# Optimization experiments

Hardware: AMD Instinct MI355X
Metric: run time of the kernel (lower is better)

The kernel has to match this reference:

```python
import jax, jax.numpy as jnp
import numpy as np

N_NODES = 100000
N_EDGES = 3200000


def setup_inputs() -> dict:
    key = jax.random.key(0)
    ks = jax.random.split(key, 10)
    inp = {
        "x": jax.random.normal(ks[0], (N_NODES, 16), dtype=jnp.float32),
        "edge_index": jax.random.randint(ks[1], (2, N_EDGES), 0, N_NODES, dtype=jnp.int64),
        "W1": jax.random.normal(ks[2], (16, 32), dtype=jnp.float32) * 0.25,
        "b1": jax.random.normal(ks[3], (32,), dtype=jnp.float32) * 0.02,
        "W2": jax.random.normal(ks[4], (32, 32), dtype=jnp.float32) * 0.18,
        "b2": jax.random.normal(ks[5], (32,), dtype=jnp.float32) * 0.02,
        "Wl1": jax.random.normal(ks[6], (32, 32), dtype=jnp.float32) * 0.18,
        "bl1": jax.random.normal(ks[7], (32,), dtype=jnp.float32) * 0.02,
        "Wl4": jax.random.normal(ks[8], (32, 1), dtype=jnp.float32) * 0.18,
        "bl4": jax.random.normal(ks[9], (1,), dtype=jnp.float32) * 0.02,
    }
    return inp


def _gcn_norm(edge_index, n_nodes):
    # PyG GCNConv default: add self-loops, symmetric normalization D^-1/2 A_hat D^-1/2.
    loops = jnp.arange(n_nodes, dtype=edge_index.dtype)
    row = jnp.concatenate([edge_index[0], loops])  # source j
    col = jnp.concatenate([edge_index[1], loops])  # target i
    deg = jax.ops.segment_sum(jnp.ones_like(col, dtype=jnp.float32), col, num_segments=n_nodes)
    dinv = jnp.where(deg > 0, jax.lax.rsqrt(deg), 0.0)
    norm = dinv[row] * dinv[col]  # [E + N]
    return row, col, norm


def _gcn_conv(x, W, b, row, col, norm, n_nodes):
    h = x @ W                                   # [N, out] small GEMM
    msgs = h[row] * norm[:, None]               # irregular gather, [E+N, out]
    out = jax.ops.segment_sum(msgs, col, num_segments=n_nodes)  # scatter-add
    return out + b


def reference(x, edge_index, W1, b1, W2, b2, Wl1, bl1, Wl4, bl4):
    n = x.shape[0]
    row, col, norm = _gcn_norm(edge_index, n)
    h = jax.nn.relu(_gcn_conv(x, W1, b1, row, col, norm, n))
    h = jax.nn.relu(_gcn_conv(h, W2, b2, row, col, norm, n))
    h = jax.nn.relu(h @ Wl1 + bl1)
    return h @ Wl4 + bl4  # [N, 1]
```

## Files before the change

### kernel.cpp

```cpp
#include <hip/hip_runtime.h>
#include <hip/hip_fp16.h>
#include <math.h>


#define BN 256
#define BSH 8
#define NBUF 512
#define EPB 4096
#define EPT 8
#define CMAX 10240
#define SLDS 1536

__global__ void __launch_bounds__(512)
bucket_scatter(const int* __restrict__ row, const int* __restrict__ col,
               int* __restrict__ gCursor, int* __restrict__ packed,
               int E, int NB, int C) {
    __shared__ int hist[NBUF];
    __shared__ int base[NBUF];
    int t = threadIdx.x;
    int blockBase = blockIdx.x * EPB;
    for (int i = t; i < NB; i += 512) hist[i] = 0;
    __syncthreads();
    int pay[EPT];
    int meta[EPT];
#pragma unroll
    for (int k = 0; k < EPT; ++k) {
        int e = blockBase + k * 512 + t;
        if (e < E) {
            int c = col[e];
            int b = c >> BSH;
            int r = atomicAdd(&hist[b], 1);
            pay[k] = (row[e] << BSH) | (c & (BN - 1));
            meta[k] = (b << 16) | r;
        } else {
            meta[k] = -1;
        }
    }
    __syncthreads();
    for (int b = t; b < NB; b += 512) {
        int c = hist[b];
        base[b] = c ? atomicAdd(&gCursor[b], c) : 0;
    }
    __syncthreads();
#pragma unroll
    for (int k = 0; k < EPT; ++k) {
        int m = meta[k];
        if (m >= 0) {
            int b = m >> 16;
            int off = base[b] + (m & 0xFFFF);
            if (off < C)
                packed[(size_t)b * C + off] = pay[k];
        }
    }
}

__global__ void __launch_bounds__(1024)
bucket_finalize(const int* __restrict__ packed, const int* __restrict__ gCursor,
                int2* __restrict__ rowRange, int* __restrict__ rowMid,
                float* __restrict__ dinv, int* __restrict__ srcs,
                const float4* __restrict__ x4, __half* __restrict__ xs,
                int N, int C, int halfN) {
    __shared__ int cnt[BN * 2];
    __shared__ int cur[BN * 2];
    __shared__ float sdv[BN];
    __shared__ int wsum[16];
    __shared__ int sorted[CMAX];
    int bkt = blockIdx.x;
    int t = threadIdx.x;
    int nodeBase = bkt << BSH;
    if (t < BN * 2) cnt[t] = 0;
    __syncthreads();
    int beg = bkt * C;
    int end = beg + min(gCursor[bkt], C);
    int m = end - beg;
    for (int e = beg + t; e < end; e += 1024) {
        int w = packed[e];
        int key = ((w & (BN - 1)) << 1) | ((w >> BSH) >= halfN ? 1 : 0);
        atomicAdd(&cnt[key], 1);
    }
    __syncthreads();
    int c0 = (t < BN) ? cnt[2 * t] : 0;
    int c1 = (t < BN) ? cnt[2 * t + 1] : 0;
    int s = c0 + c1;
    int lane = t & 63, wv = t >> 6;
    int v = s;
#pragma unroll
    for (int off = 1; off < 64; off <<= 1) {
        int u = __shfl_up(v, off);
        if (lane >= off) v += u;
    }
    if (lane == 63) wsum[wv] = v;
    __syncthreads();
    int addv = 0;
#pragma unroll
    for (int w = 0; w < 16; ++w) addv += (w < wv) ? wsum[w] : 0;
    v += addv;
    if (t < BN) {
        int p = v - s;
        cur[2 * t] = p;
        cur[2 * t + 1] = p + c0;
        float d = rsqrtf((float)s + 1.0f);
        sdv[t] = d;
        int n = nodeBase + t;
        if (n < N) {
            rowRange[n] = make_int2(beg + p, beg + p + s);
            rowMid[n] = beg + p + c0;
            dinv[n] = d;
        }
    }
    __syncthreads();
    bool useLds = (m <= CMAX);
    for (int e = beg + t; e < end; e += 1024) {
        int w = packed[e];
        int src = w >> BSH;
        int key = ((w & (BN - 1)) << 1) | (src >= halfN ? 1 : 0);
        int pos = atomicAdd(&cur[key], 1);
        if (useLds) sorted[pos] = src;
        else        srcs[beg + pos] = src;
    }
    __syncthreads();
    if (useLds)
        for (int i = t; i < m; i += 1024) srcs[beg + i] = sorted[i];
    {
        int n = t >> 1, hf = t & 1;
        int g = nodeBase + n;
        if (t < BN * 2 && g < N) {
            float d = sdv[n];
            float4 va = x4[(size_t)g * 4 + hf * 2];
            float4 vb = x4[(size_t)g * 4 + hf * 2 + 1];
            __half2 h0 = __floats2half2_rn(va.x * d, va.y * d);
            __half2 h1 = __floats2half2_rn(va.z * d, va.w * d);
            __half2 h2 = __floats2half2_rn(vb.x * d, vb.y * d);
            __half2 h3 = __floats2half2_rn(vb.z * d, vb.w * d);
            uint4 u;
            u.x = *(unsigned*)&h0; u.y = *(unsigned*)&h1;
            u.z = *(unsigned*)&h2; u.w = *(unsigned*)&h3;
            *(uint4*)(xs + (size_t)g * 16 + hf * 8) = u;
        }
    }
}

__device__ __forceinline__ void acc8(float* a, uint4 u) {
    float2 f;
    f = __half22float2(*(const __half2*)&u.x); a[0] += f.x; a[1] += f.y;
    f = __half22float2(*(const __half2*)&u.y); a[2] += f.x; a[3] += f.y;
    f = __half22float2(*(const __half2*)&u.z); a[4] += f.x; a[5] += f.y;
    f = __half22float2(*(const __half2*)&u.w); a[6] += f.x; a[7] += f.y;
}

__device__ __forceinline__ void gather_pipe(float* a, const int* __restrict__ idx,
                                            const __half* __restrict__ tbl,
                                            int rowHalves, int off8,
                                            int first, int limit, int stride) {
    if (first >= limit) return;
    int cntE = (limit - first + stride - 1) / stride;
    int last = limit - 1;
    int i0 = idx[first];
    int i1 = idx[min(first + stride, last)];
    int i2 = idx[min(first + stride * 2, last)];
    int i3 = idx[min(first + stride * 3, last)];
    uint4 f0 = *(const uint4*)(tbl + (size_t)i0 * rowHalves + off8 * 8);
    uint4 f1 = *(const uint4*)(tbl + (size_t)i1 * rowHalves + off8 * 8);
    uint4 f2 = *(const uint4*)(tbl + (size_t)i2 * rowHalves + off8 * 8);
    uint4 f3 = *(const uint4*)(tbl + (size_t)i3 * rowHalves + off8 * 8);
    int i = 0;
    for (; i + 4 <= cntE; i += 4) {
        int n0 = idx[min(first + stride * (i + 4), last)];
        int n1 = idx[min(first + stride * (i + 5), last)];
        int n2 = idx[min(first + stride * (i + 6), last)];
        int n3 = idx[min(first + stride * (i + 7), last)];
        acc8(a, f0); f0 = *(const uint4*)(tbl + (size_t)n0 * rowHalves + off8 * 8);
        acc8(a, f1); f1 = *(const uint4*)(tbl + (size_t)n1 * rowHalves + off8 * 8);
        acc8(a, f2); f2 = *(const uint4*)(tbl + (size_t)n2 * rowHalves + off8 * 8);
        acc8(a, f3); f3 = *(const uint4*)(tbl + (size_t)n3 * rowHalves + off8 * 8);
    }
    int r = cntE - i;
    if (r > 0) acc8(a, f0);
    if (r > 1) acc8(a, f1);
    if (r > 2) acc8(a, f2);
}

__global__ void __launch_bounds__(256)
gather_conv1(const int2* __restrict__ rowRange, const int* __restrict__ srcs,
             const __half* __restrict__ xs, const float* __restrict__ dinv,
             const float* __restrict__ W1, const float* __restrict__ b1,
             __half* __restrict__ hs1, int N) {
    __shared__ float A[32][17];
    __shared__ float sW[512];
    __shared__ float sb[32];
    __shared__ int sIdx[SLDS];
    int t = threadIdx.x;
    for (int i = t; i < 512; i += 256) sW[i] = W1[i];
    if (t < 32) sb[t] = b1[t];
    int node0 = blockIdx.x * 32;
    int lastN = min(node0 + 31, N - 1);
    int base = rowRange[node0].x;
    int tot = rowRange[lastN].y - base;
    bool useLds = (tot <= SLDS);
    if (useLds)
        for (int i = t; i < tot; i += 256) sIdx[i] = srcs[base + i];
    __syncthreads();
    int tt = blockIdx.x * 256 + t;
    int node = tt >> 3, q = tt & 7, ln = t >> 3;
    int eo = q >> 1, hf = q & 1;
    float a[8] = {0.f, 0.f, 0.f, 0.f, 0.f, 0.f, 0.f, 0.f};
    float di = 0.f;
    if (node < N) {
        int2 rr = rowRange[node];
        if (useLds)
            gather_pipe(a, sIdx, xs, 16, hf, rr.x - base + eo, rr.y - base, 4);
        else
            gather_pipe(a, srcs, xs, 16, hf, rr.x + eo, rr.y, 4);
        if (eo == 0)
            acc8(a, *(const uint4*)(xs + (size_t)node * 16 + hf * 8));
        di = dinv[node];
    }
#pragma unroll
    for (int j = 0; j < 8; ++j) {
        a[j] += __shfl_xor(a[j], 2);
        a[j] += __shfl_xor(a[j], 4);
        a[j] *= di;
    }
    if (eo == 0) {
#pragma unroll
        for (int j = 0; j < 8; ++j) A[ln][hf * 8 + j] = a[j];
    }
    __syncthreads();
    if (node < N) {
        int k0 = q * 4;
        float acc[4];
#pragma unroll
        for (int j = 0; j < 4; ++j) acc[j] = sb[k0 + j];
#pragma unroll
        for (int c = 0; c < 16; ++c) {
            float ac = A[ln][c];
#pragma unroll
            for (int j = 0; j < 4; ++j) acc[j] += ac * sW[c * 32 + k0 + j];
        }
        __half2 h0 = __floats2half2_rn(di * fmaxf(acc[0], 0.f),
                                       di * fmaxf(acc[1], 0.f));
        __half2 h1 = __floats2half2_rn(di * fmaxf(acc[2], 0.f),
                                       di * fmaxf(acc[3], 0.f));
        uint2 u;
        u.x = *(unsigned*)&h0; u.y = *(unsigned*)&h1;
        *(uint2*)(hs1 + (size_t)node * 32 + k0) = u;
    }
}

__global__ void __launch_bounds__(256)
gather_conv2_lo(const int2* __restrict__ rowRange, const int* __restrict__ rowMid,
                const int* __restrict__ srcs, const __half* __restrict__ hs1,
                float* __restrict__ A2, int N) {
    __shared__ int sIdx[SLDS];
    int t = threadIdx.x;
    int node0 = blockIdx.x * 32;
    int lastN = min(node0 + 31, N - 1);
    int base = rowRange[node0].x;
    int tot = rowRange[lastN].y - base;
    bool useLds = (tot <= SLDS);
    if (useLds)
        for (int i = t; i < tot; i += 256) sIdx[i] = srcs[base + i];
    __syncthreads();
    int tt = blockIdx.x * 256 + t;
    int node = tt >> 3, q = tt & 7;
    int eo = q >> 2, part = q & 3;
    float a[8] = {0.f, 0.f, 0.f, 0.f, 0.f, 0.f, 0.f, 0.f};
    if (node < N) {
        int beg = rowRange[node].x, mid = rowMid[node];
        if (useLds)
            gather_pipe(a, sIdx, hs1, 32, part, beg - base + eo, mid - base, 2);
        else
            gather_pipe(a, srcs, hs1, 32, part, beg + eo, mid, 2);
    }
#pragma unroll
    for (int j = 0; j < 8; ++j) a[j] += __shfl_xor(a[j], 4);
    if (node < N && eo == 0) {
        float4 r0, r1;
        r0.x = a[0]; r0.y = a[1]; r0.z = a[2]; r0.w = a[3];
        r1.x = a[4]; r1.y = a[5]; r1.z = a[6]; r1.w = a[7];
        *(float4*)(A2 + (size_t)node * 32 + part * 8) = r0;
        *(float4*)(A2 + (size_t)node * 32 + part * 8 + 4) = r1;
    }
}

__global__ void __launch_bounds__(256)
gather_conv2_hi_head(const int2* __restrict__ rowRange, const int* __restrict__ rowMid,
                     const int* __restrict__ srcs, const __half* __restrict__ hs1,
                     const float* __restrict__ A2, const float* __restrict__ dinv,
                     const float* __restrict__ W2, const float* __restrict__ b2,
                     const float* __restrict__ Wl1, const float* __restrict__ bl1,
                     const float* __restrict__ Wl4, const float* __restrict__ bl4,
                     float* __restrict__ out, int N) {
    __shared__ float A[32][33];
    __shared__ float sW2[1024];
    __shared__ float sWl1[1024];
    __shared__ float sb2[32], sbl1[32], sWl4[32];
    __shared__ float sbl4;
    __shared__ int sIdx[SLDS];
    int t = threadIdx.x;
    for (int i = t; i < 1024; i += 256) { sW2[i] = W2[i]; sWl1[i] = Wl1[i]; }
    if (t < 32) { sb2[t] = b2[t]; sbl1[t] = bl1[t]; sWl4[t] = Wl4[t]; }
    if (t == 0) sbl4 = bl4[0];
    int node0 = blockIdx.x * 32;
    int lastN = min(node0 + 31, N - 1);
    int base = rowRange[node0].x;
    int tot = rowRange[lastN].y - base;
    bool useLds = (tot <= SLDS);
    if (useLds)
        for (int i = t; i < tot; i += 256) sIdx[i] = srcs[base + i];
    __syncthreads();
    int tt = blockIdx.x * 256 + t;
    int node = tt >> 3, q = tt & 7, ln = t >> 3;
    int eo = q >> 2, part = q & 3;
    float a[8] = {0.f, 0.f, 0.f, 0.f, 0.f, 0.f, 0.f, 0.f};
    if (node < N) {
        int mid = rowMid[node], end = rowRange[node].y;
        if (useLds)
            gather_pipe(a, sIdx, hs1, 32, part, mid - base + eo, end - base, 2);
        else
            gather_pipe(a, srcs, hs1, 32, part, mid + eo, end, 2);
        if (eo == 0)
            acc8(a, *(const uint4*)(hs1 + (size_t)node * 32 + part * 8));
    }
#pragma unroll
    for (int j = 0; j < 8; ++j) a[j] += __shfl_xor(a[j], 4);
    if (node < N && eo == 0) {
        float4 l0 = *(const float4*)(A2 + (size_t)node * 32 + part * 8);
        float4 l1 = *(const float4*)(A2 + (size_t)node * 32 + part * 8 + 4);
        a[0] += l0.x; a[1] += l0.y; a[2] += l0.z; a[3] += l0.w;
        a[4] += l1.x; a[5] += l1.y; a[6] += l1.z; a[7] += l1.w;
        float di = dinv[node];
#pragma unroll
        for (int j = 0; j < 8; ++j) a[j] *= di;
#pragma unroll
        for (int j = 0; j < 8; ++j) A[ln][part * 8 + j] = a[j];
    }
    __syncthreads();
    int k0 = q * 4;
    float h2[4];
#pragma unroll
    for (int j = 0; j < 4; ++j) h2[j] = sb2[k0 + j];
#pragma unroll
    for (int c = 0; c < 32; ++c) {
        float ac = A[ln][c];
#pragma unroll
        for (int j = 0; j < 4; ++j) h2[j] += ac * sW2[c * 32 + k0 + j];
    }
#pragma unroll
    for (int j = 0; j < 4; ++j) h2[j] = fmaxf(h2[j], 0.f);
    __syncthreads();
#pragma unroll
    for (int j = 0; j < 4; ++j) A[ln][k0 + j] = h2[j];
    __syncthreads();
    float h3[4];
#pragma unroll
    for (int j = 0; j < 4; ++j) h3[j] = sbl1[k0 + j];
#pragma unroll
    for (int c = 0; c < 32; ++c) {
        float ac = A[ln][c];
#pragma unroll
        for (int j = 0; j < 4; ++j) h3[j] += ac * sWl1[c * 32 + k0 + j];
    }
    float p = 0.f;
#pragma unroll
    for (int j = 0; j < 4; ++j) p += fmaxf(h3[j], 0.f) * sWl4[k0 + j];
    p += __shfl_xor(p, 1);
    p += __shfl_xor(p, 2);
    p += __shfl_xor(p, 4);
    if (q == 0 && node < N) out[node] = p + sbl4;
}

extern "C" void kernel_launch(void* const* d_in, const int* in_sizes, int n_in,
                              void* d_out, int out_size, void* d_ws, size_t ws_size,
                              hipStream_t stream) {
    const float* x   = (const float*)d_in[0];
    const int*   ei  = (const int*)d_in[1];
    const float* W1  = (const float*)d_in[2];
    const float* b1  = (const float*)d_in[3];
    const float* W2  = (const float*)d_in[4];
    const float* b2  = (const float*)d_in[5];
    const float* Wl1 = (const float*)d_in[6];
    const float* bl1 = (const float*)d_in[7];
    const float* Wl4 = (const float*)d_in[8];
    const float* bl4 = (const float*)d_in[9];
    float* out = (float*)d_out;

    const int N = in_sizes[0] / 16;
    const int E = in_sizes[1] / 2;
    const int* row = ei;
    const int* col = ei + E;
    const int NB = (N + BN - 1) >> BSH;
    const int halfN = N / 2;
    int C = (E + NB - 1) / NB;
    C = (C * 9 + 7) / 8;
    C = (C + 63) & ~63;

    char* ws = (char*)d_ws;
    auto align = [](size_t v) { return (v + 511) & ~(size_t)511; };
    size_t o = 0;
    int*    gCursor  = (int*)(ws + o);    o = align(o + (size_t)NBUF * 4);
    int2*   rowRange = (int2*)(ws + o);   o = align(o + (size_t)N * 8);
    int*    rowMid   = (int*)(ws + o);    o = align(o + (size_t)N * 4);
    float*  dinv     = (float*)(ws + o);  o = align(o + (size_t)N * 4);
    int*    packed   = (int*)(ws + o);    o = align(o + (size_t)NB * C * 4);
    int*    srcs     = (int*)(ws + o);    o = align(o + (size_t)NB * C * 4);
    __half* xs       = (__half*)(ws + o); o = align(o + (size_t)N * 16 * 2);
    __half* hs1      = (__half*)(ws + o); o = align(o + (size_t)N * 32 * 2);
    float*  A2       = (float*)(ws + o);  o = align(o + (size_t)N * 32 * 4);

    const int BLK = 256;
    int gridSc = (E + EPB - 1) / EPB;
    int gridG8 = (N * 8 + BLK - 1) / BLK;

    hipMemsetAsync(gCursor, 0, (size_t)NBUF * 4, stream);
    bucket_scatter<<<gridSc, 512, 0, stream>>>(row, col, gCursor, packed, E, NB, C);
    bucket_finalize<<<NB, 1024, 0, stream>>>(packed, gCursor, rowRange, rowMid, dinv,
                                             srcs, (const float4*)x, xs, N, C, halfN);

    gather_conv1<<<gridG8, BLK, 0, stream>>>(rowRange, srcs, xs, dinv, W1, b1, hs1, N);

    gather_conv2_lo<<<gridG8, BLK, 0, stream>>>(rowRange, rowMid, srcs, hs1, A2, N);
    gather_conv2_hi_head<<<gridG8, BLK, 0, stream>>>(rowRange, rowMid, srcs, hs1, A2,
                                                     dinv, W2, b2, Wl1, bl1,
                                                     Wl4, bl4, out, N);
}
```

Baseline: 196.6 us.

## Merge split conv2 gather passes into a single fused gather-head kernel

Removes the source-half partitioning of edges within each destination node, along with the rowMid array and the intermediate A2 buffer. Conv2 aggregation now runs in one kernel that gathers all neighbours and applies the MLP head directly. This eliminates a kernel launch, the fp32 partial-sum round trip and the duplicated index loads. The trade-off is that gathers span the whole hs1 feature table instead of half of it at a time, which may reduce L2 cache hit rates.

```diff
diff --git a/kernel.cpp b/kernel.cpp
--- a/kernel.cpp
+++ b/kernel.cpp
@@ -56,32 +56,29 @@
 
 __global__ void __launch_bounds__(1024)
 bucket_finalize(const int* __restrict__ packed, const int* __restrict__ gCursor,
-                int2* __restrict__ rowRange, int* __restrict__ rowMid,
-                float* __restrict__ dinv, int* __restrict__ srcs,
+                int2* __restrict__ rowRange, float* __restrict__ dinv,
+                int* __restrict__ srcs,
                 const float4* __restrict__ x4, __half* __restrict__ xs,
-                int N, int C, int halfN) {
-    __shared__ int cnt[BN * 2];
-    __shared__ int cur[BN * 2];
+                int N, int C) {
+    __shared__ int cnt[BN];
+    __shared__ int cur[BN];
     __shared__ float sdv[BN];
     __shared__ int wsum[16];
     __shared__ int sorted[CMAX];
     int bkt = blockIdx.x;
     int t = threadIdx.x;
     int nodeBase = bkt << BSH;
-    if (t < BN * 2) cnt[t] = 0;
+    if (t < BN) cnt[t] = 0;
     __syncthreads();
     int beg = bkt * C;
     int end = beg + min(gCursor[bkt], C);
     int m = end - beg;
     for (int e = beg + t; e < end; e += 1024) {
         int w = packed[e];
-        int key = ((w & (BN - 1)) << 1) | ((w >> BSH) >= halfN ? 1 : 0);
-        atomicAdd(&cnt[key], 1);
-    }
-    __syncthreads();
-    int c0 = (t < BN) ? cnt[2 * t] : 0;
-    int c1 = (t < BN) ? cnt[2 * t + 1] : 0;
-    int s = c0 + c1;
+        atomicAdd(&cnt[w & (BN - 1)], 1);
+    }
+    __syncthreads();
+    int s = (t < BN) ? cnt[t] : 0;
     int lane = t & 63, wv = t >> 6;
     int v = s;
 #pragma unroll
@@ -97,14 +94,12 @@
     v += addv;
     if (t < BN) {
         int p = v - s;
-        cur[2 * t] = p;
-        cur[2 * t + 1] = p + c0;
+        cur[t] = p;
         float d = rsqrtf((float)s + 1.0f);
         sdv[t] = d;
         int n = nodeBase + t;
         if (n < N) {
             rowRange[n] = make_int2(beg + p, beg + p + s);
-            rowMid[n] = beg + p + c0;
             dinv[n] = d;
         }
     }
@@ -113,8 +108,7 @@
     for (int e = beg + t; e < end; e += 1024) {
         int w = packed[e];
         int src = w >> BSH;
-        int key = ((w & (BN - 1)) << 1) | (src >= halfN ? 1 : 0);
-        int pos = atomicAdd(&cur[key], 1);
+        int pos = atomicAdd(&cur[w & (BN - 1)], 1);
         if (useLds) sorted[pos] = src;
         else        srcs[beg + pos] = src;
     }
@@ -248,49 +242,12 @@
 }
 
 __global__ void __launch_bounds__(256)
-gather_conv2_lo(const int2* __restrict__ rowRange, const int* __restrict__ rowMid,
-                const int* __restrict__ srcs, const __half* __restrict__ hs1,
-                float* __restrict__ A2, int N) {
-    __shared__ int sIdx[SLDS];
-    int t = threadIdx.x;
-    int node0 = blockIdx.x * 32;
-    int lastN = min(node0 + 31, N - 1);
-    int base = rowRange[node0].x;
-    int tot = rowRange[lastN].y - base;
-    bool useLds = (tot <= SLDS);
-    if (useLds)
-        for (int i = t; i < tot; i += 256) sIdx[i] = srcs[base + i];
-    __syncthreads();
-    int tt = blockIdx.x * 256 + t;
-    int node = tt >> 3, q = tt & 7;
-    int eo = q >> 2, part = q & 3;
-    float a[8] = {0.f, 0.f, 0.f, 0.f, 0.f, 0.f, 0.f, 0.f};
-    if (node < N) {
-        int beg = rowRange[node].x, mid = rowMid[node];
-        if (useLds)
-            gather_pipe(a, sIdx, hs1, 32, part, beg - base + eo, mid - base, 2);
-        else
-            gather_pipe(a, srcs, hs1, 32, part, beg + eo, mid, 2);
-    }
-#pragma unroll
-    for (int j = 0; j < 8; ++j) a[j] += __shfl_xor(a[j], 4);
-    if (node < N && eo == 0) {
-        float4 r0, r1;
-        r0.x = a[0]; r0.y = a[1]; r0.z = a[2]; r0.w = a[3];
-        r1.x = a[4]; r1.y = a[5]; r1.z = a[6]; r1.w = a[7];
-        *(float4*)(A2 + (size_t)node * 32 + part * 8) = r0;
-        *(float4*)(A2 + (size_t)node * 32 + part * 8 + 4) = r1;
-    }
-}
-
-__global__ void __launch_bounds__(256)
-gather_conv2_hi_head(const int2* __restrict__ rowRange, const int* __restrict__ rowMid,
-                     const int* __restrict__ srcs, const __half* __restrict__ hs1,
-                     const float* __restrict__ A2, const float* __restrict__ dinv,
-                     const float* __restrict__ W2, const float* __restrict__ b2,
-                     const float* __restrict__ Wl1, const float* __restrict__ bl1,
-                     const float* __restrict__ Wl4, const float* __restrict__ bl4,
-                     float* __restrict__ out, int N) {
+gather_conv2_head(const int2* __restrict__ rowRange, const int* __restrict__ srcs,
+                  const __half* __restrict__ hs1, const float* __restrict__ dinv,
+                  const float* __restrict__ W2, const float* __restrict__ b2,
+                  const float* __restrict__ Wl1, const float* __restrict__ bl1,
+                  const float* __restrict__ Wl4, const float* __restrict__ bl4,
+                  float* __restrict__ out, int N) {
     __shared__ float A[32][33];
     __shared__ float sW2[1024];
     __shared__ float sWl1[1024];
@@ -314,21 +271,17 @@
     int eo = q >> 2, part = q & 3;
     float a[8] = {0.f, 0.f, 0.f, 0.f, 0.f, 0.f, 0.f, 0.f};
     if (node < N) {
-        int mid = rowMid[node], end = rowRange[node].y;
+        int2 rr = rowRange[node];
         if (useLds)
-            gather_pipe(a, sIdx, hs1, 32, part, mid - base + eo, end - base, 2);
+            gather_pipe(a, sIdx, hs1, 32, part, rr.x - base + eo, rr.y - base, 2);
         else
-            gather_pipe(a, srcs, hs1, 32, part, mid + eo, end, 2);
+            gather_pipe(a, srcs, hs1, 32, part, rr.x + eo, rr.y, 2);
         if (eo == 0)
             acc8(a, *(const uint4*)(hs1 + (size_t)node * 32 + part * 8));
     }
 #pragma unroll
     for (int j = 0; j < 8; ++j) a[j] += __shfl_xor(a[j], 4);
     if (node < N && eo == 0) {
-        float4 l0 = *(const float4*)(A2 + (size_t)node * 32 + part * 8);
-        float4 l1 = *(const float4*)(A2 + (size_t)node * 32 + part * 8 + 4);
-        a[0] += l0.x; a[1] += l0.y; a[2] += l0.z; a[3] += l0.w;
-        a[4] += l1.x; a[5] += l1.y; a[6] += l1.z; a[7] += l1.w;
         float di = dinv[node];
 #pragma unroll
         for (int j = 0; j < 8; ++j) a[j] *= di;
@@ -390,7 +343,6 @@
     const int* row = ei;
     const int* col = ei + E;
     const int NB = (N + BN - 1) >> BSH;
-    const int halfN = N / 2;
     int C = (E + NB - 1) / NB;
     C = (C * 9 + 7) / 8;
     C = (C + 63) & ~63;
@@ -400,13 +352,11 @@
     size_t o = 0;
     int*    gCursor  = (int*)(ws + o);    o = align(o + (size_t)NBUF * 4);
     int2*   rowRange = (int2*)(ws + o);   o = align(o + (size_t)N * 8);
-    int*    rowMid   = (int*)(ws + o);    o = align(o + (size_t)N * 4);
     float*  dinv     = (float*)(ws + o);  o = align(o + (size_t)N * 4);
     int*    packed   = (int*)(ws + o);    o = align(o + (size_t)NB * C * 4);
     int*    srcs     = (int*)(ws + o);    o = align(o + (size_t)NB * C * 4);
     __half* xs       = (__half*)(ws + o); o = align(o + (size_t)N * 16 * 2);
     __half* hs1      = (__half*)(ws + o); o = align(o + (size_t)N * 32 * 2);
-    float*  A2       = (float*)(ws + o);  o = align(o + (size_t)N * 32 * 4);
 
     const int BLK = 256;
     int gridSc = (E + EPB - 1) / EPB;
@@ -414,13 +364,12 @@
 
     hipMemsetAsync(gCursor, 0, (size_t)NBUF * 4, stream);
     bucket_scatter<<<gridSc, 512, 0, stream>>>(row, col, gCursor, packed, E, NB, C);
-    bucket_finalize<<<NB, 1024, 0, stream>>>(packed, gCursor, rowRange, rowMid, dinv,
-                                             srcs, (const float4*)x, xs, N, C, halfN);
+    bucket_finalize<<<NB, 1024, 0, stream>>>(packed, gCursor, rowRange, dinv,
+                                             srcs, (const float4*)x, xs, N, C);
 
     gather_conv1<<<gridG8, BLK, 0, stream>>>(rowRange, srcs, xs, dinv, W1, b1, hs1, N);
 
-    gather_conv2_lo<<<gridG8, BLK, 0, stream>>>(rowRange, rowMid, srcs, hs1, A2, N);
-    gather_conv2_hi_head<<<gridG8, BLK, 0, stream>>>(rowRange, rowMid, srcs, hs1, A2,
-                                                     dinv, W2, b2, Wl1, bl1,
-                                                     Wl4, bl4, out, N);
-}
+    gather_conv2_head<<<gridG8, BLK, 0, stream>>>(rowRange, srcs, hs1, dinv,
+                                                  W2, b2, Wl1, bl1,
+                                                  Wl4, bl4, out, N);
+}
```

Result: faster. 187.6 us (-4.6%).
